# Kernel tuning notes

Hardware: AMD Instinct MI355X
Metric: run time of the kernel (lower is better)

Reference implementation:

```python
import jax, jax.numpy as jnp
import numpy as np

DMODEL = 512
NUM_HEADS = 8
HEAD_DIM = DMODEL // NUM_HEADS


def setup_inputs() -> dict:
    key = jax.random.key(0)
    k1, k2, k3, k4, k5 = jax.random.split(key, 5)
    x = jax.random.normal(k1, (4, 2048, DMODEL), dtype=jnp.float32)
    s = 1.0 / np.sqrt(DMODEL)
    W_qkv = jax.random.uniform(k2, (DMODEL, 3 * DMODEL), jnp.float32, -s, s)
    b_qkv = jax.random.uniform(k3, (3 * DMODEL,), jnp.float32, -s, s)
    W_out = jax.random.uniform(k4, (DMODEL, DMODEL), jnp.float32, -s, s)
    b_out = jax.random.uniform(k5, (DMODEL,), jnp.float32, -s, s)
    return {"x": x, "W_qkv": W_qkv, "b_qkv": b_qkv, "W_out": W_out, "b_out": b_out}


def reference(x, W_qkv, b_qkv, W_out, b_out):
    B, T, D = x.shape
    H, Hd = NUM_HEADS, HEAD_DIM
    qkv = x @ W_qkv + b_qkv                      # [B, T, 3D]
    qkv = qkv.reshape(B, T, 3, H, Hd).transpose(2, 0, 3, 1, 4)  # [3, B, H, T, Hd]
    q, k, v = qkv[0], qkv[1], qkv[2]
    scores = jnp.einsum('bhqd,bhkd->bhqk', q, k) / np.sqrt(Hd)  # [B, H, T, T]
    causal = jnp.tril(jnp.ones((T, T), dtype=bool))
    scores = jnp.where(causal, scores, -jnp.inf)
    weights = jax.nn.softmax(scores, axis=-1)
    out = jnp.einsum('bhqk,bhkd->bhqd', weights, v)  # [B, H, T, Hd]
    out = out.transpose(0, 2, 1, 3).reshape(B, T, D)
    return out @ W_out + b_out
```

## Files before the change

kernel.cpp:

```cpp
#include <hip/hip_runtime.h>
#include <cstdint>
#include <cstddef>

#define D_MODEL 512
#define SEQ_T 2048
#define NHEADS 8
#define HDIM 64

typedef __attribute__((ext_vector_type(8))) short bf16x8;
typedef __attribute__((ext_vector_type(4))) float f32x4;

__device__ __forceinline__ unsigned short f2bf(float f) {
  unsigned int u = __float_as_uint(f);
  u += 0x7FFFu + ((u >> 16) & 1u);
  return (unsigned short)(u >> 16);
}

__device__ __forceinline__ unsigned int pack_bf16(float lo, float hi) {
  unsigned int a = __float_as_uint(lo) + 0x8000u;
  unsigned int b = __float_as_uint(hi) + 0x8000u;
  return __builtin_amdgcn_perm(b, a, 0x07060302u);
}

#define QSCALE 0.18033688011112043f
#define SSHIFT 16.0f

__device__ __forceinline__ void async_lds16(const unsigned short* g,
                                            unsigned short* l) {
  __builtin_amdgcn_global_load_lds(
      (const __attribute__((address_space(1))) void*)g,
      (__attribute__((address_space(3))) void*)l, 16, 0, 0);
}

__global__ __launch_bounds__(256) void prep_kernel(
    const float* __restrict__ x, const float* __restrict__ W_qkv,
    const float* __restrict__ W_out, unsigned short* __restrict__ xb,
    unsigned short* __restrict__ Wqkt, unsigned short* __restrict__ Wot) {
  __shared__ float tile[64][65];
  const int bid = blockIdx.x;
  if (bid < 2048) {
    int i = (bid * 256 + threadIdx.x) * 8;
    float4 a = *(const float4*)(x + i);
    float4 b = *(const float4*)(x + i + 4);
    ushort4 lo = {f2bf(a.x), f2bf(a.y), f2bf(a.z), f2bf(a.w)};
    ushort4 hi = {f2bf(b.x), f2bf(b.y), f2bf(b.z), f2bf(b.w)};
    *(ushort4*)(xb + i) = lo;
    *(ushort4*)(xb + i + 4) = hi;
    return;
  }
  const float* src;
  unsigned short* dst;
  int R = 512, C, c0, r0;
  if (bid < 2048 + 192) {
    int t = bid - 2048;
    C = 1536; c0 = (t % 24) * 64; r0 = (t / 24) * 64;
    src = W_qkv; dst = Wqkt;
  } else {
    int t = bid - 2240;
    C = 512; c0 = (t & 7) * 64; r0 = (t >> 3) * 64;
    src = W_out; dst = Wot;
  }
  for (int i = threadIdx.x; i < 64 * 64; i += 256) {
    int r = i >> 6, c = i & 63;
    tile[r][c] = src[(size_t)(r0 + r) * C + c0 + c];
  }
  __syncthreads();
  for (int i = threadIdx.x; i < 64 * 64; i += 256) {
    int c = i >> 6, r = i & 63;
    dst[(size_t)(c0 + c) * R + r0 + r] = f2bf(tile[r][c]);
  }
}

__global__ __launch_bounds__(256) void gemm_qkv_mfma(
    const unsigned short* __restrict__ xb, const unsigned short* __restrict__ Wt,
    const float* __restrict__ bias, unsigned short* __restrict__ Qb,
    unsigned short* __restrict__ Kb, unsigned short* __restrict__ Vtb) {
  __shared__ unsigned short As[128 * 32];
  __shared__ unsigned short Bs[128 * 32];
  const int tid = threadIdx.x;
  const int w = tid >> 6, lane = tid & 63;
  const int quad = lane >> 4, l15 = lane & 15;
  const int wm = w >> 1, wn = w & 1;
  const int m0 = blockIdx.x * 128, n0 = blockIdx.y * 128;

  const unsigned short* ga = xb + (size_t)(m0 + (tid >> 2)) * 512 + (tid & 3) * 8;
  const unsigned short* gb = Wt + (size_t)(n0 + (tid >> 2)) * 512 + (tid & 3) * 8;
  unsigned short* lA = As + tid * 8;
  unsigned short* lB = Bs + tid * 8;

  f32x4 acc[4][4] = {};
  for (int k0 = 0; k0 < 512; k0 += 32) {
    async_lds16(ga + k0, lA);
    async_lds16(ga + 64 * 512 + k0, lA + 2048);
    async_lds16(gb + k0, lB);
    async_lds16(gb + 64 * 512 + k0, lB + 2048);
    __syncthreads();
    bf16x8 af[4], bfr[4];
#pragma unroll
    for (int mb = 0; mb < 4; ++mb)
      af[mb] = *(const bf16x8*)&As[(wm * 64 + mb * 16 + l15) * 32 + quad * 8];
#pragma unroll
    for (int nb = 0; nb < 4; ++nb)
      bfr[nb] = *(const bf16x8*)&Bs[(wn * 64 + nb * 16 + l15) * 32 + quad * 8];
#pragma unroll
    for (int mb = 0; mb < 4; ++mb)
#pragma unroll
      for (int nb = 0; nb < 4; ++nb)
        acc[mb][nb] = __builtin_amdgcn_mfma_f32_16x16x32_bf16(
            af[mb], bfr[nb], acc[mb][nb], 0, 0, 0);
    __syncthreads();
  }

  const int cbase = n0 + wn * 64;
  const int three = cbase >> 9;
  const int h = (cbase >> 6) & 7;
  const int bh = ((m0 >> 11) << 3) + h;
  const int t0 = (m0 & 2047) + wm * 64;
  float bv[4];
#pragma unroll
  for (int nb = 0; nb < 4; ++nb) bv[nb] = bias[cbase + nb * 16 + l15];

  if (three == 2) {
#pragma unroll
    for (int mb = 0; mb < 4; ++mb)
#pragma unroll
      for (int nb = 0; nb < 4; ++nb) {
        int trow = t0 + mb * 16 + quad * 4;
        ushort4 v = {f2bf(acc[mb][nb][0] + bv[nb]), f2bf(acc[mb][nb][1] + bv[nb]),
                     f2bf(acc[mb][nb][2] + bv[nb]), f2bf(acc[mb][nb][3] + bv[nb])};
        *(ushort4*)(Vtb + ((size_t)bh * HDIM + nb * 16 + l15) * SEQ_T + trow) = v;
      }
  } else {
    unsigned short* dst = three ? Kb : Qb;
    const float sc = three ? 1.0f : QSCALE;
#pragma unroll
    for (int mb = 0; mb < 4; ++mb)
#pragma unroll
      for (int nb = 0; nb < 4; ++nb)
#pragma unroll
        for (int r = 0; r < 4; ++r) {
          int trow = t0 + mb * 16 + quad * 4 + r;
          dst[((size_t)bh * SEQ_T + trow) * HDIM + nb * 16 + l15] =
              f2bf((acc[mb][nb][r] + bv[nb]) * sc);
        }
  }
}

__global__ __launch_bounds__(256, 4) void attn_mfma4(
    const unsigned short* __restrict__ Qb, const unsigned short* __restrict__ Kb,
    const unsigned short* __restrict__ Vtb, unsigned short* __restrict__ AOb) {
  __shared__ __align__(16) unsigned short Ks[2][64 * 64];
  __shared__ __align__(16) unsigned short Vs[2][64 * 64];
  __shared__ __align__(16) unsigned short Pt[4][16 * 64];
  const int tid = threadIdx.x;
  const int w = tid >> 6, lane = tid & 63;
  const int quad = lane >> 4, l15 = lane & 15;

  const int bid = blockIdx.x;
  const int xcd = bid & 7;
  const int ii = bid >> 3;
  const int bh = xcd + 8 * (ii & 3);
  const int qt = 31 - (ii >> 2);

  const unsigned short* kbase = Kb + (size_t)bh * SEQ_T * HDIM;
  const unsigned short* vbase = Vtb + (size_t)bh * HDIM * SEQ_T;
  const int sr = tid >> 3;
  const int lc = tid & 7;
  const int scol = lc * 8;
  const int swc = (lc ^ (sr & 7)) * 8;

  const unsigned short* qp =
      Qb + ((size_t)bh * SEQ_T + qt * 64 + w * 16 + l15) * HDIM + quad * 8;
  bf16x8 qf0 = *(const bf16x8*)qp;
  bf16x8 qf1 = *(const bf16x8*)(qp + 32);

  f32x4 O[4] = {{0.f, 0.f, 0.f, 0.f}, {0.f, 0.f, 0.f, 0.f},
                {0.f, 0.f, 0.f, 0.f}, {0.f, 0.f, 0.f, 0.f}};
  float l_i = 0.f;
  const int q_rel = w * 16 + l15;
  const int r7 = l15 & 7;

  uint4 rk0, rk1, rv0, rv1;
  {
    const unsigned short* kp = kbase + (size_t)sr * 64 + scol;
    rk0 = *(const uint4*)kp;
    rk1 = *(const uint4*)(kp + 32 * 64);
    const unsigned short* vp = vbase + (size_t)sr * SEQ_T + scol;
    rv0 = *(const uint4*)vp;
    rv1 = *(const uint4*)(vp + 32 * SEQ_T);
  }
  *(uint4*)&Ks[0][sr * 64 + swc] = rk0;
  *(uint4*)&Ks[0][(sr + 32) * 64 + swc] = rk1;
  *(uint4*)&Vs[0][sr * 64 + swc] = rv0;
  *(uint4*)&Vs[0][(sr + 32) * 64 + swc] = rv1;
  __syncthreads();

  for (int i = 0; i <= qt; ++i) {
    const int cur = i & 1;
    const bool diag = (i == qt);

    if (i < qt) {
      const int nkt = i + 1;
      const unsigned short* kp = kbase + (size_t)(nkt * 64 + sr) * 64 + scol;
      rk0 = *(const uint4*)kp;
      rk1 = *(const uint4*)(kp + 32 * 64);
      const unsigned short* vp = vbase + (size_t)sr * SEQ_T + nkt * 64 + scol;
      rv0 = *(const uint4*)vp;
      rv1 = *(const uint4*)(vp + 32 * SEQ_T);
    }

    const int nb_lim = diag ? (w + 1) : 4;
    f32x4 S[4];
#pragma unroll
    for (int nb = 0; nb < 4; ++nb) {
      if (nb < nb_lim) {
        const int row = nb * 16 + l15;
        const unsigned short* k0p = &Ks[cur][row * 64 + ((quad ^ r7) * 8)];
        const unsigned short* k1p = &Ks[cur][row * 64 + (((quad + 4) ^ r7) * 8)];
        f32x4 z = {0.f, 0.f, 0.f, 0.f};
        z = __builtin_amdgcn_mfma_f32_16x16x32_bf16(*(const bf16x8*)k0p, qf0,
                                                    z, 0, 0, 0);
        S[nb] = __builtin_amdgcn_mfma_f32_16x16x32_bf16(*(const bf16x8*)k1p,
                                                        qf1, z, 0, 0, 0);
      }
    }

#pragma unroll
    for (int nb = 0; nb < 4; ++nb) {
      if (nb < nb_lim) {
        float pp[4];
#pragma unroll
        for (int r = 0; r < 4; ++r) {
          float p = __builtin_amdgcn_exp2f(S[nb][r] - SSHIFT);
          if (diag) {
            int key_rel = nb * 16 + quad * 4 + r;
            if (key_rel > q_rel) p = 0.f;
          }
          pp[r] = p;
          l_i += p;
        }
        int c = 2 * nb + (quad >> 1);
        uint2 pk = {pack_bf16(pp[0], pp[1]), pack_bf16(pp[2], pp[3])};
        *(uint2*)&Pt[w][l15 * 64 + ((c ^ r7) * 8) + (quad & 1) * 4] = pk;
      } else {
        int c = 2 * nb + (quad >> 1);
        uint2 z2 = {0u, 0u};
        *(uint2*)&Pt[w][l15 * 64 + ((c ^ r7) * 8) + (quad & 1) * 4] = z2;
      }
    }

    const int kpv = (!diag || w >= 2) ? 2 : 1;
    bf16x8 pb0 = *(const bf16x8*)&Pt[w][l15 * 64 + ((quad ^ r7) * 8)];
    bf16x8 pb1 = *(const bf16x8*)&Pt[w][l15 * 64 + (((quad + 4) ^ r7) * 8)];
#pragma unroll
    for (int nbd = 0; nbd < 4; ++nbd) {
      const int row = nbd * 16 + l15;
      const unsigned short* v0p = &Vs[cur][row * 64 + ((quad ^ r7) * 8)];
      O[nbd] = __builtin_amdgcn_mfma_f32_16x16x32_bf16(*(const bf16x8*)v0p,
                                                       pb0, O[nbd], 0, 0, 0);
      if (kpv == 2) {
        const unsigned short* v1p =
            &Vs[cur][row * 64 + (((quad + 4) ^ r7) * 8)];
        O[nbd] = __builtin_amdgcn_mfma_f32_16x16x32_bf16(*(const bf16x8*)v1p,
                                                         pb1, O[nbd], 0, 0, 0);
      }
    }

    if (i < qt) {
      const int nxt = cur ^ 1;
      *(uint4*)&Ks[nxt][sr * 64 + swc] = rk0;
      *(uint4*)&Ks[nxt][(sr + 32) * 64 + swc] = rk1;
      *(uint4*)&Vs[nxt][sr * 64 + swc] = rv0;
      *(uint4*)&Vs[nxt][(sr + 32) * 64 + swc] = rv1;
      __syncthreads();
    }
  }

  float lt = l_i;
  lt += __shfl_xor(lt, 16);
  lt += __shfl_xor(lt, 32);
  float inv = 1.0f / lt;
  const int bb = bh >> 3, h = bh & 7;
  int qrow = qt * 64 + q_rel;
  unsigned short* dst = AOb + ((size_t)bb * SEQ_T + qrow) * D_MODEL + (h << 6);
#pragma unroll
  for (int nbd = 0; nbd < 4; ++nbd) {
    ushort4 o4 = {f2bf(O[nbd][0] * inv), f2bf(O[nbd][1] * inv),
                  f2bf(O[nbd][2] * inv), f2bf(O[nbd][3] * inv)};
    *(ushort4*)(dst + nbd * 16 + quad * 4) = o4;
  }
}

__global__ __launch_bounds__(256) void gemm_out_mfma(
    const unsigned short* __restrict__ AOb, const unsigned short* __restrict__ Wot,
    const float* __restrict__ bias, float* __restrict__ out) {
  __shared__ unsigned short As[128 * 32];
  __shared__ unsigned short Bs[128 * 32];
  const int tid = threadIdx.x;
  const int w = tid >> 6, lane = tid & 63;
  const int quad = lane >> 4, l15 = lane & 15;
  const int wm = w >> 1, wn = w & 1;
  const int m0 = blockIdx.x * 128, n0 = blockIdx.y * 128;

  const unsigned short* ga = AOb + (size_t)(m0 + (tid >> 2)) * 512 + (tid & 3) * 8;
  const unsigned short* gb = Wot + (size_t)(n0 + (tid >> 2)) * 512 + (tid & 3) * 8;
  unsigned short* lA = As + tid * 8;
  unsigned short* lB = Bs + tid * 8;

  f32x4 acc[4][4] = {};
  for (int k0 = 0; k0 < 512; k0 += 32) {
    async_lds16(ga + k0, lA);
    async_lds16(ga + 64 * 512 + k0, lA + 2048);
    async_lds16(gb + k0, lB);
    async_lds16(gb + 64 * 512 + k0, lB + 2048);
    __syncthreads();
    bf16x8 af[4], bfr[4];
#pragma unroll
    for (int mb = 0; mb < 4; ++mb)
      af[mb] = *(const bf16x8*)&As[(wm * 64 + mb * 16 + l15) * 32 + quad * 8];
#pragma unroll
    for (int nb = 0; nb < 4; ++nb)
      bfr[nb] = *(const bf16x8*)&Bs[(wn * 64 + nb * 16 + l15) * 32 + quad * 8];
#pragma unroll
    for (int mb = 0; mb < 4; ++mb)
#pragma unroll
      for (int nb = 0; nb < 4; ++nb)
        acc[mb][nb] = __builtin_amdgcn_mfma_f32_16x16x32_bf16(
            af[mb], bfr[nb], acc[mb][nb], 0, 0, 0);
    __syncthreads();
  }

  const int cbase = n0 + wn * 64;
  const int rbase = m0 + wm * 64;
  float bv[4];
#pragma unroll
  for (int nb = 0; nb < 4; ++nb) bv[nb] = bias[cbase + nb * 16 + l15];
#pragma unroll
  for (int mb = 0; mb < 4; ++mb)
#pragma unroll
    for (int nb = 0; nb < 4; ++nb)
#pragma unroll
      for (int r = 0; r < 4; ++r)
        out[(size_t)(rbase + mb * 16 + quad * 4 + r) * 512 + cbase + nb * 16 +
            l15] = acc[mb][nb][r] + bv[nb];
}

extern "C" void kernel_launch(void* const* d_in, const int* in_sizes, int n_in,
                              void* d_out, int out_size, void* d_ws,
                              size_t ws_size, hipStream_t stream) {
  const float* x     = (const float*)d_in[0];
  const float* W_qkv = (const float*)d_in[1];
  const float* b_qkv = (const float*)d_in[2];
  const float* W_out = (const float*)d_in[3];
  const float* b_out = (const float*)d_in[4];
  float* out = (float*)d_out;

  const size_t NX = (size_t)4 * SEQ_T * D_MODEL;
  unsigned short* xb   = (unsigned short*)d_ws;
  unsigned short* Wqkt = xb + NX;
  unsigned short* Wot  = Wqkt + (size_t)1536 * 512;
  unsigned short* Qb   = Wot + (size_t)512 * 512;
  unsigned short* Kb   = Qb + NX;
  unsigned short* Vtb  = Kb + NX;
  unsigned short* AOb  = Vtb + NX;

  prep_kernel<<<2304, 256, 0, stream>>>(x, W_qkv, W_out, xb, Wqkt, Wot);
  gemm_qkv_mfma<<<dim3(64, 12), 256, 0, stream>>>(xb, Wqkt, b_qkv, Qb, Kb, Vtb);
  attn_mfma4<<<dim3(1024), 256, 0, stream>>>(Qb, Kb, Vtb, AOb);
  gemm_out_mfma<<<dim3(64, 4), 256, 0, stream>>>(AOb, Wot, b_out, out);
}
```

Before: 157.7 us.

## Widen GEMM K-tiles with swizzled LDS, restructure attention loop and row-sum via MFMA

Both GEMMs now load 64-wide K slices into XOR-swizzled LDS, which halves the barrier count and avoids bank conflicts. The output GEMM switches to 64x128 tiles so it launches twice as many blocks. The attention kernel peels the diagonal tile out of the main loop so full tiles run without masking branches. It computes the softmax denominator with an MFMA against a ones vector instead of scalar adds and shuffles, and reorders the query-tile schedule to balance causal work. Q is now written transposed and gathered with strided scalar loads, which makes the initial Q load more expensive.

```diff
diff --git a/kernel.cpp b/kernel.cpp
--- a/kernel.cpp
+++ b/kernel.cpp
@@ -73,41 +73,59 @@
 
 __global__ __launch_bounds__(256) void gemm_qkv_mfma(
     const unsigned short* __restrict__ xb, const unsigned short* __restrict__ Wt,
-    const float* __restrict__ bias, unsigned short* __restrict__ Qb,
+    const float* __restrict__ bias, unsigned short* __restrict__ Qtb,
     unsigned short* __restrict__ Kb, unsigned short* __restrict__ Vtb) {
-  __shared__ unsigned short As[128 * 32];
-  __shared__ unsigned short Bs[128 * 32];
+  __shared__ unsigned short As[128 * 64];
+  __shared__ unsigned short Bs[128 * 64];
   const int tid = threadIdx.x;
   const int w = tid >> 6, lane = tid & 63;
   const int quad = lane >> 4, l15 = lane & 15;
   const int wm = w >> 1, wn = w & 1;
   const int m0 = blockIdx.x * 128, n0 = blockIdx.y * 128;
 
-  const unsigned short* ga = xb + (size_t)(m0 + (tid >> 2)) * 512 + (tid & 3) * 8;
-  const unsigned short* gb = Wt + (size_t)(n0 + (tid >> 2)) * 512 + (tid & 3) * 8;
+  const int srow = tid >> 3;
+  const int schunk = (tid & 7) ^ (srow & 7);
+  const unsigned short* ga = xb + (size_t)(m0 + srow) * 512 + schunk * 8;
+  const unsigned short* gb = Wt + (size_t)(n0 + srow) * 512 + schunk * 8;
   unsigned short* lA = As + tid * 8;
   unsigned short* lB = Bs + tid * 8;
 
   f32x4 acc[4][4] = {};
-  for (int k0 = 0; k0 < 512; k0 += 32) {
-    async_lds16(ga + k0, lA);
-    async_lds16(ga + 64 * 512 + k0, lA + 2048);
-    async_lds16(gb + k0, lB);
-    async_lds16(gb + 64 * 512 + k0, lB + 2048);
+  for (int k0 = 0; k0 < 512; k0 += 64) {
+#pragma unroll
+    for (int rr = 0; rr < 4; ++rr) {
+      async_lds16(ga + (size_t)rr * 32 * 512 + k0, lA + rr * 2048);
+      async_lds16(gb + (size_t)rr * 32 * 512 + k0, lB + rr * 2048);
+    }
     __syncthreads();
-    bf16x8 af[4], bfr[4];
+    bf16x8 af[4][2], bfr[4][2];
+#pragma unroll
+    for (int mb = 0; mb < 4; ++mb) {
+      int row = wm * 64 + mb * 16 + l15;
+#pragma unroll
+      for (int kk = 0; kk < 2; ++kk) {
+        int slot = (kk * 4 + quad) ^ (row & 7);
+        af[mb][kk] = *(const bf16x8*)&As[row * 64 + slot * 8];
+      }
+    }
+#pragma unroll
+    for (int nb = 0; nb < 4; ++nb) {
+      int row = wn * 64 + nb * 16 + l15;
+#pragma unroll
+      for (int kk = 0; kk < 2; ++kk) {
+        int slot = (kk * 4 + quad) ^ (row & 7);
+        bfr[nb][kk] = *(const bf16x8*)&Bs[row * 64 + slot * 8];
+      }
+    }
 #pragma unroll
     for (int mb = 0; mb < 4; ++mb)
-      af[mb] = *(const bf16x8*)&As[(wm * 64 + mb * 16 + l15) * 32 + quad * 8];
-#pragma unroll
-    for (int nb = 0; nb < 4; ++nb)
-      bfr[nb] = *(const bf16x8*)&Bs[(wn * 64 + nb * 16 + l15) * 32 + quad * 8];
-#pragma unroll
-    for (int mb = 0; mb < 4; ++mb)
-#pragma unroll
-      for (int nb = 0; nb < 4; ++nb)
+#pragma unroll
+      for (int nb = 0; nb < 4; ++nb) {
         acc[mb][nb] = __builtin_amdgcn_mfma_f32_16x16x32_bf16(
-            af[mb], bfr[nb], acc[mb][nb], 0, 0, 0);
+            af[mb][0], bfr[nb][0], acc[mb][nb], 0, 0, 0);
+        acc[mb][nb] = __builtin_amdgcn_mfma_f32_16x16x32_bf16(
+            af[mb][1], bfr[nb][1], acc[mb][nb], 0, 0, 0);
+      }
     __syncthreads();
   }
 
@@ -120,7 +138,19 @@
 #pragma unroll
   for (int nb = 0; nb < 4; ++nb) bv[nb] = bias[cbase + nb * 16 + l15];
 
-  if (three == 2) {
+  if (three == 0) {
+#pragma unroll
+    for (int mb = 0; mb < 4; ++mb)
+#pragma unroll
+      for (int nb = 0; nb < 4; ++nb) {
+        int trow = t0 + mb * 16 + quad * 4;
+        ushort4 v = {f2bf((acc[mb][nb][0] + bv[nb]) * QSCALE),
+                     f2bf((acc[mb][nb][1] + bv[nb]) * QSCALE),
+                     f2bf((acc[mb][nb][2] + bv[nb]) * QSCALE),
+                     f2bf((acc[mb][nb][3] + bv[nb]) * QSCALE)};
+        *(ushort4*)(Qtb + ((size_t)bh * HDIM + nb * 16 + l15) * SEQ_T + trow) = v;
+      }
+  } else if (three == 2) {
 #pragma unroll
     for (int mb = 0; mb < 4; ++mb)
 #pragma unroll
@@ -131,8 +161,6 @@
         *(ushort4*)(Vtb + ((size_t)bh * HDIM + nb * 16 + l15) * SEQ_T + trow) = v;
       }
   } else {
-    unsigned short* dst = three ? Kb : Qb;
-    const float sc = three ? 1.0f : QSCALE;
 #pragma unroll
     for (int mb = 0; mb < 4; ++mb)
 #pragma unroll
@@ -140,14 +168,14 @@
 #pragma unroll
         for (int r = 0; r < 4; ++r) {
           int trow = t0 + mb * 16 + quad * 4 + r;
-          dst[((size_t)bh * SEQ_T + trow) * HDIM + nb * 16 + l15] =
-              f2bf((acc[mb][nb][r] + bv[nb]) * sc);
+          Kb[((size_t)bh * SEQ_T + trow) * HDIM + nb * 16 + l15] =
+              f2bf(acc[mb][nb][r] + bv[nb]);
         }
   }
 }
 
-__global__ __launch_bounds__(256, 4) void attn_mfma4(
-    const unsigned short* __restrict__ Qb, const unsigned short* __restrict__ Kb,
+__global__ __launch_bounds__(256, 4) void attn_mfma5(
+    const unsigned short* __restrict__ Qtb, const unsigned short* __restrict__ Kb,
     const unsigned short* __restrict__ Vtb, unsigned short* __restrict__ AOb) {
   __shared__ __align__(16) unsigned short Ks[2][64 * 64];
   __shared__ __align__(16) unsigned short Vs[2][64 * 64];
@@ -158,9 +186,12 @@
 
   const int bid = blockIdx.x;
   const int xcd = bid & 7;
-  const int ii = bid >> 3;
-  const int bh = xcd + 8 * (ii & 3);
-  const int qt = 31 - (ii >> 2);
+  const int j = bid >> 3;
+  const int c = j & 31, g = j >> 5;
+  const int k = c >> 2;
+  const int bh = xcd + 8 * (c & 3);
+  const int qt = (g == 0) ? (31 - k) : (g == 1) ? (16 + k)
+               : (g == 2) ? (15 - k) : k;
 
   const unsigned short* kbase = Kb + (size_t)bh * SEQ_T * HDIM;
   const unsigned short* vbase = Vtb + (size_t)bh * HDIM * SEQ_T;
@@ -169,14 +200,25 @@
   const int scol = lc * 8;
   const int swc = (lc ^ (sr & 7)) * 8;
 
-  const unsigned short* qp =
-      Qb + ((size_t)bh * SEQ_T + qt * 64 + w * 16 + l15) * HDIM + quad * 8;
-  bf16x8 qf0 = *(const bf16x8*)qp;
-  bf16x8 qf1 = *(const bf16x8*)(qp + 32);
+  bf16x8 qf0, qf1;
+  {
+    unsigned short qraw[16];
+    const unsigned short* qp =
+        Qtb + ((size_t)bh * HDIM + quad * 8) * SEQ_T + qt * 64 + w * 16 + l15;
+#pragma unroll
+    for (int jj = 0; jj < 8; ++jj) {
+      qraw[jj] = qp[(size_t)jj * SEQ_T];
+      qraw[8 + jj] = qp[(size_t)(32 + jj) * SEQ_T];
+    }
+    qf0 = *(const bf16x8*)qraw;
+    qf1 = *(const bf16x8*)(qraw + 8);
+  }
+  const short oneb = (short)0x3F80;
+  const bf16x8 ones = {oneb, oneb, oneb, oneb, oneb, oneb, oneb, oneb};
 
   f32x4 O[4] = {{0.f, 0.f, 0.f, 0.f}, {0.f, 0.f, 0.f, 0.f},
                 {0.f, 0.f, 0.f, 0.f}, {0.f, 0.f, 0.f, 0.f}};
-  float l_i = 0.f;
+  f32x4 l_acc = {0.f, 0.f, 0.f, 0.f};
   const int q_rel = w * 16 + l15;
   const int r7 = l15 & 7;
 
@@ -195,11 +237,9 @@
   *(uint4*)&Vs[0][(sr + 32) * 64 + swc] = rv1;
   __syncthreads();
 
-  for (int i = 0; i <= qt; ++i) {
+  for (int i = 0; i < qt; ++i) {
     const int cur = i & 1;
-    const bool diag = (i == qt);
-
-    if (i < qt) {
+    {
       const int nkt = i + 1;
       const unsigned short* kp = kbase + (size_t)(nkt * 64 + sr) * 64 + scol;
       rk0 = *(const uint4*)kp;
@@ -209,14 +249,64 @@
       rv1 = *(const uint4*)(vp + 32 * SEQ_T);
     }
 
-    const int nb_lim = diag ? (w + 1) : 4;
+    f32x4 S[4];
+#pragma unroll
+    for (int nb = 0; nb < 4; ++nb) {
+      const int row = nb * 16 + l15;
+      const unsigned short* k0p = &Ks[cur][row * 64 + ((quad ^ r7) * 8)];
+      const unsigned short* k1p = &Ks[cur][row * 64 + (((quad + 4) ^ r7) * 8)];
+      f32x4 z = {0.f, 0.f, 0.f, 0.f};
+      z = __builtin_amdgcn_mfma_f32_16x16x32_bf16(*(const bf16x8*)k0p, qf0, z,
+                                                  0, 0, 0);
+      S[nb] = __builtin_amdgcn_mfma_f32_16x16x32_bf16(*(const bf16x8*)k1p, qf1,
+                                                      z, 0, 0, 0);
+    }
+
+#pragma unroll
+    for (int nb = 0; nb < 4; ++nb) {
+      float p0 = __builtin_amdgcn_exp2f(S[nb][0] - SSHIFT);
+      float p1 = __builtin_amdgcn_exp2f(S[nb][1] - SSHIFT);
+      float p2 = __builtin_amdgcn_exp2f(S[nb][2] - SSHIFT);
+      float p3 = __builtin_amdgcn_exp2f(S[nb][3] - SSHIFT);
+      int cc = 2 * nb + (quad >> 1);
+      uint2 pk = {pack_bf16(p0, p1), pack_bf16(p2, p3)};
+      *(uint2*)&Pt[w][l15 * 64 + ((cc ^ r7) * 8) + (quad & 1) * 4] = pk;
+    }
+
+    bf16x8 pb0 = *(const bf16x8*)&Pt[w][l15 * 64 + ((quad ^ r7) * 8)];
+    bf16x8 pb1 = *(const bf16x8*)&Pt[w][l15 * 64 + (((quad + 4) ^ r7) * 8)];
+    l_acc = __builtin_amdgcn_mfma_f32_16x16x32_bf16(ones, pb0, l_acc, 0, 0, 0);
+    l_acc = __builtin_amdgcn_mfma_f32_16x16x32_bf16(ones, pb1, l_acc, 0, 0, 0);
+#pragma unroll
+    for (int nbd = 0; nbd < 4; ++nbd) {
+      const int row = nbd * 16 + l15;
+      const unsigned short* v0p = &Vs[cur][row * 64 + ((quad ^ r7) * 8)];
+      const unsigned short* v1p = &Vs[cur][row * 64 + (((quad + 4) ^ r7) * 8)];
+      O[nbd] = __builtin_amdgcn_mfma_f32_16x16x32_bf16(*(const bf16x8*)v0p, pb0,
+                                                       O[nbd], 0, 0, 0);
+      O[nbd] = __builtin_amdgcn_mfma_f32_16x16x32_bf16(*(const bf16x8*)v1p, pb1,
+                                                       O[nbd], 0, 0, 0);
+    }
+
+    const int nxt = cur ^ 1;
+    *(uint4*)&Ks[nxt][sr * 64 + swc] = rk0;
+    *(uint4*)&Ks[nxt][(sr + 32) * 64 + swc] = rk1;
+    *(uint4*)&Vs[nxt][sr * 64 + swc] = rv0;
+    *(uint4*)&Vs[nxt][(sr + 32) * 64 + swc] = rv1;
+    __syncthreads();
+  }
+
+  {
+    const int cur = qt & 1;
+    const int nb_lim = w + 1;
     f32x4 S[4];
 #pragma unroll
     for (int nb = 0; nb < 4; ++nb) {
       if (nb < nb_lim) {
         const int row = nb * 16 + l15;
         const unsigned short* k0p = &Ks[cur][row * 64 + ((quad ^ r7) * 8)];
-        const unsigned short* k1p = &Ks[cur][row * 64 + (((quad + 4) ^ r7) * 8)];
+        const unsigned short* k1p =
+            &Ks[cur][row * 64 + (((quad + 4) ^ r7) * 8)];
         f32x4 z = {0.f, 0.f, 0.f, 0.f};
         z = __builtin_amdgcn_mfma_f32_16x16x32_bf16(*(const bf16x8*)k0p, qf0,
                                                     z, 0, 0, 0);
@@ -224,40 +314,37 @@
                                                         qf1, z, 0, 0, 0);
       }
     }
-
 #pragma unroll
     for (int nb = 0; nb < 4; ++nb) {
+      int cc = 2 * nb + (quad >> 1);
       if (nb < nb_lim) {
         float pp[4];
 #pragma unroll
         for (int r = 0; r < 4; ++r) {
           float p = __builtin_amdgcn_exp2f(S[nb][r] - SSHIFT);
-          if (diag) {
-            int key_rel = nb * 16 + quad * 4 + r;
-            if (key_rel > q_rel) p = 0.f;
-          }
-          pp[r] = p;
-          l_i += p;
+          int key_rel = nb * 16 + quad * 4 + r;
+          pp[r] = (key_rel > q_rel) ? 0.f : p;
         }
-        int c = 2 * nb + (quad >> 1);
         uint2 pk = {pack_bf16(pp[0], pp[1]), pack_bf16(pp[2], pp[3])};
-        *(uint2*)&Pt[w][l15 * 64 + ((c ^ r7) * 8) + (quad & 1) * 4] = pk;
+        *(uint2*)&Pt[w][l15 * 64 + ((cc ^ r7) * 8) + (quad & 1) * 4] = pk;
       } else {
-        int c = 2 * nb + (quad >> 1);
         uint2 z2 = {0u, 0u};
-        *(uint2*)&Pt[w][l15 * 64 + ((c ^ r7) * 8) + (quad & 1) * 4] = z2;
-      }
-    }
-
-    const int kpv = (!diag || w >= 2) ? 2 : 1;
+        *(uint2*)&Pt[w][l15 * 64 + ((cc ^ r7) * 8) + (quad & 1) * 4] = z2;
+      }
+    }
+    const int kpv = (w >= 2) ? 2 : 1;
     bf16x8 pb0 = *(const bf16x8*)&Pt[w][l15 * 64 + ((quad ^ r7) * 8)];
     bf16x8 pb1 = *(const bf16x8*)&Pt[w][l15 * 64 + (((quad + 4) ^ r7) * 8)];
+    l_acc = __builtin_amdgcn_mfma_f32_16x16x32_bf16(ones, pb0, l_acc, 0, 0, 0);
+    if (kpv == 2)
+      l_acc =
+          __builtin_amdgcn_mfma_f32_16x16x32_bf16(ones, pb1, l_acc, 0, 0, 0);
 #pragma unroll
     for (int nbd = 0; nbd < 4; ++nbd) {
       const int row = nbd * 16 + l15;
       const unsigned short* v0p = &Vs[cur][row * 64 + ((quad ^ r7) * 8)];
-      O[nbd] = __builtin_amdgcn_mfma_f32_16x16x32_bf16(*(const bf16x8*)v0p,
-                                                       pb0, O[nbd], 0, 0, 0);
+      O[nbd] = __builtin_amdgcn_mfma_f32_16x16x32_bf16(*(const bf16x8*)v0p, pb0,
+                                                       O[nbd], 0, 0, 0);
       if (kpv == 2) {
         const unsigned short* v1p =
             &Vs[cur][row * 64 + (((quad + 4) ^ r7) * 8)];
@@ -265,21 +352,9 @@
                                                          pb1, O[nbd], 0, 0, 0);
       }
     }
-
-    if (i < qt) {
-      const int nxt = cur ^ 1;
-      *(uint4*)&Ks[nxt][sr * 64 + swc] = rk0;
-      *(uint4*)&Ks[nxt][(sr + 32) * 64 + swc] = rk1;
-      *(uint4*)&Vs[nxt][sr * 64 + swc] = rv0;
-      *(uint4*)&Vs[nxt][(sr + 32) * 64 + swc] = rv1;
-      __syncthreads();
-    }
-  }
-
-  float lt = l_i;
-  lt += __shfl_xor(lt, 16);
-  lt += __shfl_xor(lt, 32);
-  float inv = 1.0f / lt;
+  }
+
+  float inv = 1.0f / l_acc[0];
   const int bb = bh >> 3, h = bh & 7;
   int qrow = qt * 64 + q_rel;
   unsigned short* dst = AOb + ((size_t)bb * SEQ_T + qrow) * D_MODEL + (h << 6);
@@ -294,54 +369,71 @@
 __global__ __launch_bounds__(256) void gemm_out_mfma(
     const unsigned short* __restrict__ AOb, const unsigned short* __restrict__ Wot,
     const float* __restrict__ bias, float* __restrict__ out) {
-  __shared__ unsigned short As[128 * 32];
-  __shared__ unsigned short Bs[128 * 32];
+  __shared__ unsigned short As[64 * 64];
+  __shared__ unsigned short Bs[128 * 64];
   const int tid = threadIdx.x;
   const int w = tid >> 6, lane = tid & 63;
   const int quad = lane >> 4, l15 = lane & 15;
-  const int wm = w >> 1, wn = w & 1;
-  const int m0 = blockIdx.x * 128, n0 = blockIdx.y * 128;
-
-  const unsigned short* ga = AOb + (size_t)(m0 + (tid >> 2)) * 512 + (tid & 3) * 8;
-  const unsigned short* gb = Wot + (size_t)(n0 + (tid >> 2)) * 512 + (tid & 3) * 8;
+  const int m0 = blockIdx.x * 64, n0 = blockIdx.y * 128;
+
+  const int srow = tid >> 3;
+  const int schunk = (tid & 7) ^ (srow & 7);
+  const unsigned short* ga = AOb + (size_t)(m0 + srow) * 512 + schunk * 8;
+  const unsigned short* gb = Wot + (size_t)(n0 + srow) * 512 + schunk * 8;
   unsigned short* lA = As + tid * 8;
   unsigned short* lB = Bs + tid * 8;
 
-  f32x4 acc[4][4] = {};
-  for (int k0 = 0; k0 < 512; k0 += 32) {
-    async_lds16(ga + k0, lA);
-    async_lds16(ga + 64 * 512 + k0, lA + 2048);
-    async_lds16(gb + k0, lB);
-    async_lds16(gb + 64 * 512 + k0, lB + 2048);
+  f32x4 acc[4][2] = {};
+  for (int k0 = 0; k0 < 512; k0 += 64) {
+#pragma unroll
+    for (int rr = 0; rr < 2; ++rr)
+      async_lds16(ga + (size_t)rr * 32 * 512 + k0, lA + rr * 2048);
+#pragma unroll
+    for (int rr = 0; rr < 4; ++rr)
+      async_lds16(gb + (size_t)rr * 32 * 512 + k0, lB + rr * 2048);
     __syncthreads();
-    bf16x8 af[4], bfr[4];
+    bf16x8 af[4][2], bfr[2][2];
+#pragma unroll
+    for (int mb = 0; mb < 4; ++mb) {
+      int row = mb * 16 + l15;
+#pragma unroll
+      for (int kk = 0; kk < 2; ++kk) {
+        int slot = (kk * 4 + quad) ^ (row & 7);
+        af[mb][kk] = *(const bf16x8*)&As[row * 64 + slot * 8];
+      }
+    }
+#pragma unroll
+    for (int nb = 0; nb < 2; ++nb) {
+      int row = w * 32 + nb * 16 + l15;
+#pragma unroll
+      for (int kk = 0; kk < 2; ++kk) {
+        int slot = (kk * 4 + quad) ^ (row & 7);
+        bfr[nb][kk] = *(const bf16x8*)&Bs[row * 64 + slot * 8];
+      }
+    }
 #pragma unroll
     for (int mb = 0; mb < 4; ++mb)
-      af[mb] = *(const bf16x8*)&As[(wm * 64 + mb * 16 + l15) * 32 + quad * 8];
-#pragma unroll
-    for (int nb = 0; nb < 4; ++nb)
-      bfr[nb] = *(const bf16x8*)&Bs[(wn * 64 + nb * 16 + l15) * 32 + quad * 8];
-#pragma unroll
-    for (int mb = 0; mb < 4; ++mb)
-#pragma unroll
-      for (int nb = 0; nb < 4; ++nb)
+#pragma unroll
+      for (int nb = 0; nb < 2; ++nb) {
         acc[mb][nb] = __builtin_amdgcn_mfma_f32_16x16x32_bf16(
-            af[mb], bfr[nb], acc[mb][nb], 0, 0, 0);
+            af[mb][0], bfr[nb][0], acc[mb][nb], 0, 0, 0);
+        acc[mb][nb] = __builtin_amdgcn_mfma_f32_16x16x32_bf16(
+            af[mb][1], bfr[nb][1], acc[mb][nb], 0, 0, 0);
+      }
     __syncthreads();
   }
 
-  const int cbase = n0 + wn * 64;
-  const int rbase = m0 + wm * 64;
-  float bv[4];
-#pragma unroll
-  for (int nb = 0; nb < 4; ++nb) bv[nb] = bias[cbase + nb * 16 + l15];
+  const int cbase = n0 + w * 32;
+  float bv[2];
+#pragma unroll
+  for (int nb = 0; nb < 2; ++nb) bv[nb] = bias[cbase + nb * 16 + l15];
 #pragma unroll
   for (int mb = 0; mb < 4; ++mb)
 #pragma unroll
-    for (int nb = 0; nb < 4; ++nb)
+    for (int nb = 0; nb < 2; ++nb)
 #pragma unroll
       for (int r = 0; r < 4; ++r)
-        out[(size_t)(rbase + mb * 16 + quad * 4 + r) * 512 + cbase + nb * 16 +
+        out[(size_t)(m0 + mb * 16 + quad * 4 + r) * 512 + cbase + nb * 16 +
             l15] = acc[mb][nb][r] + bv[nb];
 }
 
@@ -359,13 +451,14 @@
   unsigned short* xb   = (unsigned short*)d_ws;
   unsigned short* Wqkt = xb + NX;
   unsigned short* Wot  = Wqkt + (size_t)1536 * 512;
-  unsigned short* Qb   = Wot + (size_t)512 * 512;
-  unsigned short* Kb   = Qb + NX;
+  unsigned short* Qtb  = Wot + (size_t)512 * 512;
+  unsigned short* Kb   = Qtb + NX;
   unsigned short* Vtb  = Kb + NX;
   unsigned short* AOb  = Vtb + NX;
 
   prep_kernel<<<2304, 256, 0, stream>>>(x, W_qkv, W_out, xb, Wqkt, Wot);
-  gemm_qkv_mfma<<<dim3(64, 12), 256, 0, stream>>>(xb, Wqkt, b_qkv, Qb, Kb, Vtb);
-  attn_mfma4<<<dim3(1024), 256, 0, stream>>>(Qb, Kb, Vtb, AOb);
-  gemm_out_mfma<<<dim3(64, 4), 256, 0, stream>>>(AOb, Wot, b_out, out);
-}
+  gemm_qkv_mfma<<<dim3(64, 12), 256, 0, stream>>>(xb, Wqkt, b_qkv, Qtb, Kb,
+                                                  Vtb);
+  attn_mfma5<<<dim3(1024), 256, 0, stream>>>(Qtb, Kb, Vtb, AOb);
+  gemm_out_mfma<<<dim3(128, 4), 256, 0, stream>>>(AOb, Wot, b_out, out);
+}
```

Measured after the change: 132.8 us. 15.8% less time.
